# Kernel optimization log

Measured on AMD Instinct MI355X. Metric: run time of the kernel, lower is better.

The kernel has to match this reference:

```python
import jax, jax.numpy as jnp
import numpy as np

N = 20000   # nodes
K = 32      # neighbors per node (kNN graph)
C = 128     # input feature dim
H = 256     # h_theta hidden/output dim
E = N * K   # edges


def setup_inputs() -> dict:
    key = jax.random.key(0)
    k1, k2, k3, k4 = jax.random.split(key, 4)
    node_features = jax.random.normal(k1, (N, C), dtype=jnp.float32)
    senders = jax.random.randint(k2, (E,), 0, N)              # neighbor node per edge
    receivers = jnp.repeat(jnp.arange(N), K)                  # center node per edge (k-NN: exactly K each)
    W1 = jax.random.normal(k3, (2 * C, H), dtype=jnp.float32) * (1.0 / np.sqrt(2 * C))
    b1 = jnp.zeros((H,), dtype=jnp.float32)
    W2 = jax.random.normal(k4, (H, H), dtype=jnp.float32) * (1.0 / np.sqrt(H))
    b2 = jnp.zeros((H,), dtype=jnp.float32)
    return {"node_features": node_features, "senders": senders, "receivers": receivers,
            "W1": W1, "b1": b1, "W2": W2, "b2": b2}


def reference(node_features, senders, receivers, W1, b1, W2, b2):
    # gather: x_v (center) and x_vp (neighbor) per edge -> [E, C]
    x_v = node_features[receivers]
    x_vp = node_features[senders]
    # edge feature: concat([x_v, x_vp - x_v]) -> [E, 2C]
    e = jnp.concatenate([x_v, x_vp - x_v], axis=-1)
    # h_theta MLP per edge -> [E, H]
    h = jnp.dot(jax.nn.relu(jnp.dot(e, W1) + b1), W2) + b2
    # max-reduce over each node's incident edges -> [N, H]
    return jax.ops.segment_max(h, receivers, num_segments=N)
```

## Files before the change

### kernel.cpp

```cpp
#include <hip/hip_runtime.h>
#include <hip/hip_bf16.h>

#define NN    20000
#define KNN   32
#define CIN   128
#define HD    256
#define EE    (NN * KNN)
#define MT    64
#define TPB   10
#define NBLK  (EE / (MT * TPB))

typedef __bf16 bf16x8_t __attribute__((ext_vector_type(8)));
typedef __bf16 bf16x4_t __attribute__((ext_vector_type(4)));
typedef float  f32x4_t  __attribute__((ext_vector_type(4)));

__device__ __forceinline__ void gload_lds16(const __bf16* g, __bf16* l) {
    __builtin_amdgcn_global_load_lds(
        (const __attribute__((address_space(1))) void*)g,
        (__attribute__((address_space(3))) void*)l, 16, 0, 0);
}

__global__ void ec_prep(const float* __restrict__ nf, const float* __restrict__ W1,
                        const float* __restrict__ W2, __bf16* __restrict__ nfb,
                        __bf16* __restrict__ w1g, __bf16* __restrict__ w2t) {
    int bid = blockIdx.x;
    if (bid < (NN * CIN) / 256) {
        int i = bid * 256 + threadIdx.x;
        nfb[i] = (__bf16)nf[i];
    } else {
        int idx = (bid - (NN * CIN) / 256) * 256 + threadIdx.x;
        int k = idx >> 8, n = idx & 255;
        float v = (k < CIN) ? (W1[k * 256 + n] - W1[(k + CIN) * 256 + n])
                            : W1[k * 256 + n];
        int kt = k >> 5, qr = (k >> 3) & 3, j = k & 7;
        w1g[(size_t)((kt * 4 + qr) * 256 + n) * 8 + j] = (__bf16)v;
        w2t[n * 256 + k] = (__bf16)W2[k * 256 + n];
    }
}

__global__ __launch_bounds__(512, 1) void ec_main(
    const __bf16* __restrict__ nfb,
    const int*   __restrict__ senders,
    const __bf16* __restrict__ w1g,
    const __bf16* __restrict__ w2t,
    const float* __restrict__ b1,
    const float* __restrict__ b2,
    float* __restrict__ out)
{
    __shared__ __attribute__((aligned(16))) __bf16 ldsW[49152];
    __shared__ __attribute__((aligned(16))) __bf16 ldsE[8192];
    __shared__ __attribute__((aligned(16))) __bf16 ldsH[16384];

    const int tid  = threadIdx.x;
    const int lane = tid & 63;
    const int wave = tid >> 6;
    const int qrow = lane >> 4;
    const int lcol = lane & 15;
    const int blk  = blockIdx.x;
    const int fsl  = wave * 32;
    const int p0 = wave * 2, p1 = wave * 2 + 1;
    const int c0 = p0 >> 2, q0 = p0 & 3;
    const int c1 = p1 >> 2, q1 = p1 & 3;

    {
        const float4* src = (const float4*)(w1g + 16384);
        float4* dst = (float4*)ldsW;
#pragma unroll
        for (int i = 0; i < 12; ++i)
            dst[i * 512 + tid] = src[i * 512 + tid];
    }

    bf16x8_t w1r[2][2];
#pragma unroll
    for (int kt = 0; kt < 2; ++kt)
#pragma unroll
        for (int mi = 0; mi < 2; ++mi)
            w1r[kt][mi] = *(const bf16x8_t*)(w1g +
                (size_t)((kt * 4 + qrow) * 256 + fsl + mi * 16 + lcol) * 8);

    bf16x8_t w2f[8][2];
#pragma unroll
    for (int kt = 0; kt < 8; ++kt)
#pragma unroll
        for (int ni = 0; ni < 2; ++ni)
            w2f[kt][ni] = *(const bf16x8_t*)(w2t + (size_t)(fsl + ni * 16 + lcol) * 256
                                                 + kt * 32 + qrow * 8);

    float4 bias1[2];
#pragma unroll
    for (int mi = 0; mi < 2; ++mi)
        bias1[mi] = *(const float4*)(b1 + fsl + mi * 16 + qrow * 4);
    float bias2[2];
#pragma unroll
    for (int ni = 0; ni < 2; ++ni)
        bias2[ni] = b2[fsl + ni * 16 + lcol];

    {
        int sidx = senders[blk * TPB * MT + lane];
        gload_lds16(nfb + (size_t)sidx * CIN + c0 * 32 + q0 * 8, ldsE + p0 * 512);
        gload_lds16(nfb + (size_t)sidx * CIN + c1 * 32 + q1 * 8, ldsE + p1 * 512);
    }
    bf16x8_t efr[2][4];
    {
        int node0 = blk * TPB * 2;
#pragma unroll
        for (int nd = 0; nd < 2; ++nd)
#pragma unroll
            for (int c = 0; c < 4; ++c)
                efr[nd][c] = *(const bf16x8_t*)(nfb + (size_t)(node0 + nd) * CIN + c * 32 + qrow * 8);
    }
    __syncthreads();

#pragma unroll 1
    for (int t = 0; t < TPB; ++t) {
        const int node0 = (blk * TPB + t) * 2;
        const bool more = (t + 1 < TPB);

        int sidxN = 0;
        if (more) sidxN = senders[(blk * TPB + t + 1) * MT + lane];

        f32x4_t acc[2][4];
#pragma unroll
        for (int mi = 0; mi < 2; ++mi)
#pragma unroll
            for (int ni = 0; ni < 4; ++ni)
                acc[mi][ni] = (f32x4_t){0.f, 0.f, 0.f, 0.f};

#pragma unroll
        for (int kt = 0; kt < 2; ++kt)
#pragma unroll
            for (int mi = 0; mi < 2; ++mi)
#pragma unroll
                for (int ni = 0; ni < 4; ++ni)
                    acc[mi][ni] = __builtin_amdgcn_mfma_f32_16x16x32_bf16(
                        w1r[kt][mi], efr[ni >> 1][kt], acc[mi][ni], 0, 0, 0);
#pragma unroll
        for (int kt = 2; kt < 4; ++kt) {
            bf16x8_t wf[2];
#pragma unroll
            for (int mi = 0; mi < 2; ++mi)
                wf[mi] = *(const bf16x8_t*)(ldsW +
                    (size_t)(((kt - 2) * 4 + qrow) * 256 + fsl + mi * 16 + lcol) * 8);
#pragma unroll
            for (int mi = 0; mi < 2; ++mi)
#pragma unroll
                for (int ni = 0; ni < 4; ++ni)
                    acc[mi][ni] = __builtin_amdgcn_mfma_f32_16x16x32_bf16(
                        wf[mi], efr[ni >> 1][kt], acc[mi][ni], 0, 0, 0);
        }
#pragma unroll
        for (int kt = 4; kt < 8; ++kt) {
            bf16x8_t wf[2], ef[4];
#pragma unroll
            for (int mi = 0; mi < 2; ++mi)
                wf[mi] = *(const bf16x8_t*)(ldsW +
                    (size_t)(((kt - 2) * 4 + qrow) * 256 + fsl + mi * 16 + lcol) * 8);
#pragma unroll
            for (int ni = 0; ni < 4; ++ni)
                ef[ni] = *(const bf16x8_t*)(ldsE +
                    (size_t)(((kt - 4) * 4 + qrow) * 64 + ni * 16 + lcol) * 8);
#pragma unroll
            for (int mi = 0; mi < 2; ++mi)
#pragma unroll
                for (int ni = 0; ni < 4; ++ni)
                    acc[mi][ni] = __builtin_amdgcn_mfma_f32_16x16x32_bf16(
                        wf[mi], ef[ni], acc[mi][ni], 0, 0, 0);
        }

        __syncthreads();

        bf16x8_t efrN[2][4];
        if (more) {
            gload_lds16(nfb + (size_t)sidxN * CIN + c0 * 32 + q0 * 8, ldsE + p0 * 512);
            gload_lds16(nfb + (size_t)sidxN * CIN + c1 * 32 + q1 * 8, ldsE + p1 * 512);
            int nn0 = node0 + 2;
#pragma unroll
            for (int nd = 0; nd < 2; ++nd)
#pragma unroll
                for (int c = 0; c < 4; ++c)
                    efrN[nd][c] = *(const bf16x8_t*)(nfb + (size_t)(nn0 + nd) * CIN + c * 32 + qrow * 8);
        }

#pragma unroll
        for (int mi = 0; mi < 2; ++mi) {
            const int f0  = fsl + mi * 16 + qrow * 4;
            const int ktp = f0 >> 5, qrp = (f0 >> 3) & 3, jh = f0 & 7;
            float4 bb = bias1[mi];
#pragma unroll
            for (int ni = 0; ni < 4; ++ni) {
                int edge = ni * 16 + lcol;
                float v0 = acc[mi][ni][0] + bb.x;
                float v1 = acc[mi][ni][1] + bb.y;
                float v2 = acc[mi][ni][2] + bb.z;
                float v3 = acc[mi][ni][3] + bb.w;
                bf16x4_t h = { (__bf16)fmaxf(v0, 0.f), (__bf16)fmaxf(v1, 0.f),
                               (__bf16)fmaxf(v2, 0.f), (__bf16)fmaxf(v3, 0.f) };
                *(bf16x4_t*)(ldsH + (size_t)((ktp * 4 + qrp) * 64 + edge) * 8 + jh) = h;
            }
        }
        __syncthreads();

        f32x4_t acc2[4][2];
#pragma unroll
        for (int mi = 0; mi < 4; ++mi)
#pragma unroll
            for (int ni = 0; ni < 2; ++ni)
                acc2[mi][ni] = (f32x4_t){0.f, 0.f, 0.f, 0.f};
#pragma unroll
        for (int kt = 0; kt < 8; ++kt) {
            bf16x8_t af[4];
#pragma unroll
            for (int mi = 0; mi < 4; ++mi)
                af[mi] = *(const bf16x8_t*)(ldsH +
                    (size_t)((kt * 4 + qrow) * 64 + mi * 16 + lcol) * 8);
#pragma unroll
            for (int mi = 0; mi < 4; ++mi)
#pragma unroll
                for (int ni = 0; ni < 2; ++ni)
                    acc2[mi][ni] = __builtin_amdgcn_mfma_f32_16x16x32_bf16(
                        af[mi], w2f[kt][ni], acc2[mi][ni], 0, 0, 0);
        }

#pragma unroll
        for (int ni = 0; ni < 2; ++ni) {
            int col = fsl + ni * 16 + lcol;
#pragma unroll
            for (int nd = 0; nd < 2; ++nd) {
                float mx = -3.402823466e38f;
#pragma unroll
                for (int h = 0; h < 2; ++h)
#pragma unroll
                    for (int r = 0; r < 4; ++r)
                        mx = fmaxf(mx, acc2[nd * 2 + h][ni][r]);
                mx = fmaxf(mx, __shfl_xor(mx, 16, 64));
                mx = fmaxf(mx, __shfl_xor(mx, 32, 64));
                if (qrow == 0)
                    out[(size_t)(node0 + nd) * HD + col] = mx + bias2[ni];
            }
        }

        if (more) {
#pragma unroll
            for (int nd = 0; nd < 2; ++nd)
#pragma unroll
                for (int c = 0; c < 4; ++c)
                    efr[nd][c] = efrN[nd][c];
        }
    }
}

extern "C" void kernel_launch(void* const* d_in, const int* in_sizes, int n_in,
                              void* d_out, int out_size, void* d_ws, size_t ws_size,
                              hipStream_t stream) {
    const float* nf      = (const float*)d_in[0];
    const int*   senders = (const int*)d_in[1];
    const float* W1 = (const float*)d_in[3];
    const float* b1 = (const float*)d_in[4];
    const float* W2 = (const float*)d_in[5];
    const float* b2 = (const float*)d_in[6];

    __bf16* w1g = (__bf16*)d_ws;
    __bf16* w2t = w1g + 256 * 256;
    __bf16* nfb = w2t + 256 * 256;

    ec_prep<<<(NN * CIN) / 256 + 256, 256, 0, stream>>>(nf, W1, W2, nfb, w1g, w2t);
    ec_main<<<NBLK, 512, 0, stream>>>(nfb, senders, w1g, w2t, b1, b2, (float*)d_out);
}
```

Measured before the change: 240.1 us.

## Precompute per-node center projection once, double-buffer neighbor gathers, repartition GEMM2

The center-node half of the first layer (x_v times (W1a - W1b)) is now computed once per node at block start and kept in LDS, instead of once for every edge. This removes half of the GEMM1 K-dimension from the per-tile loop. Neighbor feature gathers now go into two LDS buffers, and each next tile's gather is issued before the current tile's compute, with sender indices loaded up front. GEMM2 is split so each wave covers one node's 32 edges by 64 output columns, so the max-reduction no longer spans nodes. The prep kernel converts node features with float4 loads. LDS usage and register pressure go up, and the precompute path relies on each block owning exactly 20 consecutive nodes.

```diff
diff --git a/kernel.cpp b/kernel.cpp
--- a/kernel.cpp
+++ b/kernel.cpp
@@ -24,11 +24,13 @@
                         const float* __restrict__ W2, __bf16* __restrict__ nfb,
                         __bf16* __restrict__ w1g, __bf16* __restrict__ w2t) {
     int bid = blockIdx.x;
-    if (bid < (NN * CIN) / 256) {
-        int i = bid * 256 + threadIdx.x;
-        nfb[i] = (__bf16)nf[i];
+    if (bid < (NN * CIN) / 1024) {
+        int i = (bid * 256 + threadIdx.x) * 4;
+        float4 v = *(const float4*)(nf + i);
+        bf16x4_t b = { (__bf16)v.x, (__bf16)v.y, (__bf16)v.z, (__bf16)v.w };
+        *(bf16x4_t*)(nfb + i) = b;
     } else {
-        int idx = (bid - (NN * CIN) / 256) * 256 + threadIdx.x;
+        int idx = (bid - (NN * CIN) / 1024) * 256 + threadIdx.x;
         int k = idx >> 8, n = idx & 255;
         float v = (k < CIN) ? (W1[k * 256 + n] - W1[(k + CIN) * 256 + n])
                             : W1[k * 256 + n];
@@ -47,9 +49,10 @@
     const float* __restrict__ b2,
     float* __restrict__ out)
 {
-    __shared__ __attribute__((aligned(16))) __bf16 ldsW[49152];
-    __shared__ __attribute__((aligned(16))) __bf16 ldsE[8192];
+    __shared__ __attribute__((aligned(16))) __bf16 ldsW[32768];
+    __shared__ __attribute__((aligned(16))) __bf16 ldsE[2][8192];
     __shared__ __attribute__((aligned(16))) __bf16 ldsH[16384];
+    __shared__ __attribute__((aligned(16))) float  ldsY[20 * 256];
 
     const int tid  = threadIdx.x;
     const int lane = tid & 63;
@@ -58,107 +61,116 @@
     const int lcol = lane & 15;
     const int blk  = blockIdx.x;
     const int fsl  = wave * 32;
+    const int fs2  = (wave >> 1) * 64;
+    const int eh   = wave & 1;
     const int p0 = wave * 2, p1 = wave * 2 + 1;
     const int c0 = p0 >> 2, q0 = p0 & 3;
     const int c1 = p1 >> 2, q1 = p1 & 3;
 
+    int sidxAll[TPB];
+#pragma unroll
+    for (int tt = 0; tt < TPB; ++tt)
+        sidxAll[tt] = senders[(blk * TPB + tt) * MT + lane];
+
     {
-        const float4* src = (const float4*)(w1g + 16384);
+        const float4* src = (const float4*)(w1g + 32768);
         float4* dst = (float4*)ldsW;
 #pragma unroll
-        for (int i = 0; i < 12; ++i)
+        for (int i = 0; i < 8; ++i)
             dst[i * 512 + tid] = src[i * 512 + tid];
     }
 
-    bf16x8_t w1r[2][2];
-#pragma unroll
-    for (int kt = 0; kt < 2; ++kt)
-#pragma unroll
-        for (int mi = 0; mi < 2; ++mi)
-            w1r[kt][mi] = *(const bf16x8_t*)(w1g +
-                (size_t)((kt * 4 + qrow) * 256 + fsl + mi * 16 + lcol) * 8);
-
-    bf16x8_t w2f[8][2];
+    gload_lds16(nfb + (size_t)sidxAll[0] * CIN + c0 * 32 + q0 * 8, &ldsE[0][p0 * 512]);
+    gload_lds16(nfb + (size_t)sidxAll[0] * CIN + c1 * 32 + q1 * 8, &ldsE[0][p1 * 512]);
+
+    {
+        f32x4_t ay[2][2];
+#pragma unroll
+        for (int mi = 0; mi < 2; ++mi)
+#pragma unroll
+            for (int ni = 0; ni < 2; ++ni)
+                ay[mi][ni] = (f32x4_t){0.f, 0.f, 0.f, 0.f};
+        bf16x8_t xv[2][4];
+#pragma unroll
+        for (int ni = 0; ni < 2; ++ni) {
+            int ln = ni * 16 + lcol; if (ln > 19) ln = 19;
+            const __bf16* row = nfb + (size_t)(blk * 20 + ln) * CIN;
+#pragma unroll
+            for (int c = 0; c < 4; ++c)
+                xv[ni][c] = *(const bf16x8_t*)(row + c * 32 + qrow * 8);
+        }
+#pragma unroll
+        for (int kt = 0; kt < 4; ++kt) {
+            bf16x8_t wy[2];
+#pragma unroll
+            for (int mi = 0; mi < 2; ++mi)
+                wy[mi] = *(const bf16x8_t*)(w1g +
+                    (size_t)((kt * 4 + qrow) * 256 + fsl + mi * 16 + lcol) * 8);
+#pragma unroll
+            for (int mi = 0; mi < 2; ++mi)
+#pragma unroll
+                for (int ni = 0; ni < 2; ++ni)
+                    ay[mi][ni] = __builtin_amdgcn_mfma_f32_16x16x32_bf16(
+                        wy[mi], xv[ni][kt], ay[mi][ni], 0, 0, 0);
+        }
+#pragma unroll
+        for (int mi = 0; mi < 2; ++mi)
+#pragma unroll
+            for (int ni = 0; ni < 2; ++ni) {
+                int ln = ni * 16 + lcol;
+                if (ln < 20)
+                    *(f32x4_t*)(ldsY + ln * 256 + fsl + mi * 16 + qrow * 4) = ay[mi][ni];
+            }
+    }
+
+    bf16x8_t w2f[8][4];
 #pragma unroll
     for (int kt = 0; kt < 8; ++kt)
 #pragma unroll
-        for (int ni = 0; ni < 2; ++ni)
-            w2f[kt][ni] = *(const bf16x8_t*)(w2t + (size_t)(fsl + ni * 16 + lcol) * 256
+        for (int ni = 0; ni < 4; ++ni)
+            w2f[kt][ni] = *(const bf16x8_t*)(w2t + (size_t)(fs2 + ni * 16 + lcol) * 256
                                                  + kt * 32 + qrow * 8);
 
     float4 bias1[2];
 #pragma unroll
     for (int mi = 0; mi < 2; ++mi)
         bias1[mi] = *(const float4*)(b1 + fsl + mi * 16 + qrow * 4);
-    float bias2[2];
-#pragma unroll
-    for (int ni = 0; ni < 2; ++ni)
-        bias2[ni] = b2[fsl + ni * 16 + lcol];
-
-    {
-        int sidx = senders[blk * TPB * MT + lane];
-        gload_lds16(nfb + (size_t)sidx * CIN + c0 * 32 + q0 * 8, ldsE + p0 * 512);
-        gload_lds16(nfb + (size_t)sidx * CIN + c1 * 32 + q1 * 8, ldsE + p1 * 512);
-    }
-    bf16x8_t efr[2][4];
-    {
-        int node0 = blk * TPB * 2;
-#pragma unroll
-        for (int nd = 0; nd < 2; ++nd)
-#pragma unroll
-            for (int c = 0; c < 4; ++c)
-                efr[nd][c] = *(const bf16x8_t*)(nfb + (size_t)(node0 + nd) * CIN + c * 32 + qrow * 8);
-    }
+    float bias2[4];
+#pragma unroll
+    for (int ni = 0; ni < 4; ++ni)
+        bias2[ni] = b2[fs2 + ni * 16 + lcol];
+
     __syncthreads();
 
 #pragma unroll 1
     for (int t = 0; t < TPB; ++t) {
         const int node0 = (blk * TPB + t) * 2;
-        const bool more = (t + 1 < TPB);
-
-        int sidxN = 0;
-        if (more) sidxN = senders[(blk * TPB + t + 1) * MT + lane];
+        const int cur = t & 1;
+
+        if (t + 1 < TPB) {
+            const __bf16* srow = nfb + (size_t)sidxAll[t + 1] * CIN;
+            gload_lds16(srow + c0 * 32 + q0 * 8, &ldsE[1 - cur][p0 * 512]);
+            gload_lds16(srow + c1 * 32 + q1 * 8, &ldsE[1 - cur][p1 * 512]);
+        }
 
         f32x4_t acc[2][4];
 #pragma unroll
         for (int mi = 0; mi < 2; ++mi)
 #pragma unroll
             for (int ni = 0; ni < 4; ++ni)
-                acc[mi][ni] = (f32x4_t){0.f, 0.f, 0.f, 0.f};
-
-#pragma unroll
-        for (int kt = 0; kt < 2; ++kt)
-#pragma unroll
-            for (int mi = 0; mi < 2; ++mi)
-#pragma unroll
-                for (int ni = 0; ni < 4; ++ni)
-                    acc[mi][ni] = __builtin_amdgcn_mfma_f32_16x16x32_bf16(
-                        w1r[kt][mi], efr[ni >> 1][kt], acc[mi][ni], 0, 0, 0);
-#pragma unroll
-        for (int kt = 2; kt < 4; ++kt) {
-            bf16x8_t wf[2];
+                acc[mi][ni] = *(const f32x4_t*)(ldsY + (t * 2 + (ni >> 1)) * 256
+                                                + fsl + mi * 16 + qrow * 4);
+#pragma unroll
+        for (int kt = 0; kt < 4; ++kt) {
+            bf16x8_t wf[2], ef[4];
 #pragma unroll
             for (int mi = 0; mi < 2; ++mi)
                 wf[mi] = *(const bf16x8_t*)(ldsW +
-                    (size_t)(((kt - 2) * 4 + qrow) * 256 + fsl + mi * 16 + lcol) * 8);
-#pragma unroll
-            for (int mi = 0; mi < 2; ++mi)
-#pragma unroll
-                for (int ni = 0; ni < 4; ++ni)
-                    acc[mi][ni] = __builtin_amdgcn_mfma_f32_16x16x32_bf16(
-                        wf[mi], efr[ni >> 1][kt], acc[mi][ni], 0, 0, 0);
-        }
-#pragma unroll
-        for (int kt = 4; kt < 8; ++kt) {
-            bf16x8_t wf[2], ef[4];
-#pragma unroll
-            for (int mi = 0; mi < 2; ++mi)
-                wf[mi] = *(const bf16x8_t*)(ldsW +
-                    (size_t)(((kt - 2) * 4 + qrow) * 256 + fsl + mi * 16 + lcol) * 8);
+                    (size_t)((kt * 4 + qrow) * 256 + fsl + mi * 16 + lcol) * 8);
 #pragma unroll
             for (int ni = 0; ni < 4; ++ni)
-                ef[ni] = *(const bf16x8_t*)(ldsE +
-                    (size_t)(((kt - 4) * 4 + qrow) * 64 + ni * 16 + lcol) * 8);
+                ef[ni] = *(const bf16x8_t*)(&ldsE[cur][0] +
+                    (size_t)((kt * 4 + qrow) * 64 + ni * 16 + lcol) * 8);
 #pragma unroll
             for (int mi = 0; mi < 2; ++mi)
 #pragma unroll
@@ -168,18 +180,6 @@
         }
 
         __syncthreads();
-
-        bf16x8_t efrN[2][4];
-        if (more) {
-            gload_lds16(nfb + (size_t)sidxN * CIN + c0 * 32 + q0 * 8, ldsE + p0 * 512);
-            gload_lds16(nfb + (size_t)sidxN * CIN + c1 * 32 + q1 * 8, ldsE + p1 * 512);
-            int nn0 = node0 + 2;
-#pragma unroll
-            for (int nd = 0; nd < 2; ++nd)
-#pragma unroll
-                for (int c = 0; c < 4; ++c)
-                    efrN[nd][c] = *(const bf16x8_t*)(nfb + (size_t)(nn0 + nd) * CIN + c * 32 + qrow * 8);
-        }
 
 #pragma unroll
         for (int mi = 0; mi < 2; ++mi) {
@@ -200,51 +200,40 @@
         }
         __syncthreads();
 
-        f32x4_t acc2[4][2];
-#pragma unroll
-        for (int mi = 0; mi < 4; ++mi)
-#pragma unroll
-            for (int ni = 0; ni < 2; ++ni)
+        f32x4_t acc2[2][4];
+#pragma unroll
+        for (int mi = 0; mi < 2; ++mi)
+#pragma unroll
+            for (int ni = 0; ni < 4; ++ni)
                 acc2[mi][ni] = (f32x4_t){0.f, 0.f, 0.f, 0.f};
 #pragma unroll
         for (int kt = 0; kt < 8; ++kt) {
-            bf16x8_t af[4];
-#pragma unroll
-            for (int mi = 0; mi < 4; ++mi)
+            bf16x8_t af[2];
+#pragma unroll
+            for (int mi = 0; mi < 2; ++mi)
                 af[mi] = *(const bf16x8_t*)(ldsH +
-                    (size_t)((kt * 4 + qrow) * 64 + mi * 16 + lcol) * 8);
-#pragma unroll
-            for (int mi = 0; mi < 4; ++mi)
-#pragma unroll
-                for (int ni = 0; ni < 2; ++ni)
+                    (size_t)((kt * 4 + qrow) * 64 + eh * 32 + mi * 16 + lcol) * 8);
+#pragma unroll
+            for (int mi = 0; mi < 2; ++mi)
+#pragma unroll
+                for (int ni = 0; ni < 4; ++ni)
                     acc2[mi][ni] = __builtin_amdgcn_mfma_f32_16x16x32_bf16(
                         af[mi], w2f[kt][ni], acc2[mi][ni], 0, 0, 0);
         }
 
 #pragma unroll
-        for (int ni = 0; ni < 2; ++ni) {
-            int col = fsl + ni * 16 + lcol;
-#pragma unroll
-            for (int nd = 0; nd < 2; ++nd) {
-                float mx = -3.402823466e38f;
-#pragma unroll
-                for (int h = 0; h < 2; ++h)
-#pragma unroll
-                    for (int r = 0; r < 4; ++r)
-                        mx = fmaxf(mx, acc2[nd * 2 + h][ni][r]);
-                mx = fmaxf(mx, __shfl_xor(mx, 16, 64));
-                mx = fmaxf(mx, __shfl_xor(mx, 32, 64));
-                if (qrow == 0)
-                    out[(size_t)(node0 + nd) * HD + col] = mx + bias2[ni];
-            }
-        }
-
-        if (more) {
-#pragma unroll
-            for (int nd = 0; nd < 2; ++nd)
-#pragma unroll
-                for (int c = 0; c < 4; ++c)
-                    efr[nd][c] = efrN[nd][c];
+        for (int ni = 0; ni < 4; ++ni) {
+            int col = fs2 + ni * 16 + lcol;
+            float mx = -3.402823466e38f;
+#pragma unroll
+            for (int mi = 0; mi < 2; ++mi)
+#pragma unroll
+                for (int r = 0; r < 4; ++r)
+                    mx = fmaxf(mx, acc2[mi][ni][r]);
+            mx = fmaxf(mx, __shfl_xor(mx, 16, 64));
+            mx = fmaxf(mx, __shfl_xor(mx, 32, 64));
+            if (qrow == 0)
+                out[(size_t)(node0 + eh) * HD + col] = mx + bias2[ni];
         }
     }
 }
@@ -263,6 +252,6 @@
     __bf16* w2t = w1g + 256 * 256;
     __bf16* nfb = w2t + 256 * 256;
 
-    ec_prep<<<(NN * CIN) / 256 + 256, 256, 0, stream>>>(nf, W1, W2, nfb, w1g, w2t);
+    ec_prep<<<(NN * CIN) / 1024 + 256, 256, 0, stream>>>(nf, W1, W2, nfb, w1g, w2t);
     ec_main<<<NBLK, 512, 0, stream>>>(nfb, senders, w1g, w2t, b1, b2, (float*)d_out);
 }
```

Result: faster. 230.1 us (-4.2%).
